# Kernel optimization log

Hardware: AMD Instinct MI355X
Metric: run time of the kernel (lower is better)

Reference implementation:

```python
import jax, jax.numpy as jnp
import numpy as np

B, C, O, N, T, K = 4, 64, 64, 32768, 4, 9
PAD, DIL = 4, 1  # padding*dilation, dilation
SIGMA = 0.05
EPS_BN = 1e-5


def _gather_ch(x, idx):
    # x: [B, C, N], idx: [B, N] -> gather along last dim per channel
    idx3 = jnp.broadcast_to(idx[:, None, :], x.shape)
    return jnp.take_along_axis(x, idx3, axis=-1)


def _weighted_conv(x, coords, w):
    # x: [B,C,N], coords: [B,3,N], w: [O,C,K]
    xp = jnp.pad(x, ((0, 0), (0, 0), (PAD, PAD)))
    cp = jnp.pad(coords, ((0, 0), (0, 0), (PAD, PAD)))
    win_idx = jnp.arange(N)[:, None] + jnp.arange(K) * DIL  # [N, K]
    win = xp[:, :, win_idx]   # [B,C,N,K]
    cwin = cp[:, :, win_idx]  # [B,3,N,K]
    d = cwin - cwin[:, :, :, K // 2:K // 2 + 1]
    s = jnp.sum(d * d, axis=1)                    # [B,N,K]
    r = jnp.sqrt(jnp.where(s > 0, s, 1.0))
    r = jnp.where(s > 0, r, 0.0)
    wgt = jnp.maximum(1.0 - r / SIGMA, 0.0)       # [B,N,K]
    return jnp.einsum('bcnk,bnk,ock->bon', win, wgt, w)


def _bn(x, g, b):
    # training-mode BatchNorm1d over (B, N)
    m = jnp.mean(x, axis=(0, 2), keepdims=True)
    v = jnp.var(x, axis=(0, 2), keepdims=True)
    return g[None, :, None] * (x - m) * jax.lax.rsqrt(v + EPS_BN) + b[None, :, None]


def setup_inputs() -> dict:
    key = jax.random.key(0)
    ks = jax.random.split(key, 12)
    inp = jax.random.normal(ks[0], (B, C, N), dtype=jnp.float32)
    # coords in a small box so sigma=0.05 yields non-trivial weights
    multi_coords = jax.random.uniform(ks[1], (B, 3, N, T), dtype=jnp.float32) * 0.02
    indices = jax.random.randint(ks[2], (B, N, T), 0, N, dtype=jnp.int32)
    reindices = jax.random.randint(ks[3], (B, N, T), 0, N, dtype=jnp.int32)
    fan = C * K
    conv_w = jax.random.normal(ks[4], (T, O, C, K), dtype=jnp.float32) / np.sqrt(fan)
    bn_gamma = jnp.ones((T, O), dtype=jnp.float32)
    bn_beta = jnp.zeros((T, O), dtype=jnp.float32)
    fusion_w = jax.random.normal(ks[5], (O, T * O), dtype=jnp.float32) / np.sqrt(T * O)
    fusion_b = jnp.zeros((O,), dtype=jnp.float32)
    fusion_gamma = jnp.ones((O,), dtype=jnp.float32)
    fusion_beta = jnp.zeros((O,), dtype=jnp.float32)
    return {"input": inp, "multi_coords": multi_coords, "indices": indices,
            "reindices": reindices, "conv_w": conv_w, "bn_gamma": bn_gamma,
            "bn_beta": bn_beta, "fusion_w": fusion_w, "fusion_b": fusion_b,
            "fusion_gamma": fusion_gamma, "fusion_beta": fusion_beta}


def reference(input, multi_coords, indices, reindices, conv_w, bn_gamma, bn_beta,
              fusion_w, fusion_b, fusion_gamma, fusion_beta):
    outs = []
    for i in range(T):  # fixed small set of 4 Hilbert orders
        x = _gather_ch(input, indices[:, :, i])            # [B,C,N]
        x = _weighted_conv(x, multi_coords[:, :, :, i], conv_w[i])  # [B,O,N]
        x = _bn(x, bn_gamma[i], bn_beta[i])
        x = _gather_ch(x, reindices[:, :, i])
        outs.append(x)
    cat = jnp.concatenate(outs, axis=1)                    # [B, T*O, N]
    y = jnp.einsum('bcn,oc->bon', cat, fusion_w) + fusion_b[None, :, None]
    y = _bn(y, fusion_gamma, fusion_beta)
    return jax.nn.relu(y)
```

## Files before the change

### kernel.cpp

```cpp
#include <hip/hip_runtime.h>
#include <hip/hip_bf16.h>

#define BB 4
#define CC 64
#define OO 64
#define NN 32768
#define TT 4
#define KK 9
#define PADW 4
#define SIGMA 0.05f
#define EPS_BN 1e-5f

typedef __attribute__((ext_vector_type(8))) short bf16x8;
typedef __attribute__((ext_vector_type(4))) float f32x4;

__device__ __forceinline__ unsigned short f2bf(float f) {
  __hip_bfloat16 h = __float2bfloat16(f);
  return *reinterpret_cast<unsigned short*>(&h);
}
__device__ __forceinline__ unsigned int pkbf(float a, float b) {
  float2 t; t.x = a; t.y = b;
  __hip_bfloat162 h = __float22bfloat162_rn(t);
  unsigned int r;
  __builtin_memcpy(&r, &h, 4);
  return r;
}

__global__ __launch_bounds__(256) void prep_kernel(
    const float* __restrict__ inp, unsigned short* __restrict__ xTb,
    const float* __restrict__ cw,  unsigned short* __restrict__ W4,
    const int*   __restrict__ ind, const float* __restrict__ mc,
    int* __restrict__ indT, float* __restrict__ mcT)
{
  __shared__ float xt[64][65];
  const int bid = blockIdx.x;
  const int tid = threadIdx.x;

  if (bid < 2048) {
    const int n0 = (bid & 511) * 64;
    const int b  = bid >> 9;
    {
      int nl = tid & 63, c4 = tid >> 6;
      #pragma unroll
      for (int i = 0; i < 16; ++i) {
        int c = c4 * 16 + i;
        xt[c][nl] = inp[((size_t)(b*CC + c))*NN + n0 + nl];
      }
    }
    __syncthreads();
    {
      int nl = tid >> 2, cq = tid & 3;
      unsigned int pk[8];
      #pragma unroll
      for (int i = 0; i < 8; ++i) {
        int c = cq*16 + i*2;
        pk[i] = pkbf(xt[c][nl], xt[c+1][nl]);
      }
      unsigned int* dst = (unsigned int*)(xTb + (((size_t)b*NN) + n0 + nl)*CC + cq*16);
      ((int4*)dst)[0] = make_int4((int)pk[0],(int)pk[1],(int)pk[2],(int)pk[3]);
      ((int4*)dst)[1] = make_int4((int)pk[4],(int)pk[5],(int)pk[6],(int)pk[7]);
    }
  } else if (bid < 2560) {
    const int id = bid - 2048;
    const int n  = (id & 127) * 256 + tid;
    const int b  = id >> 7;
    int4 iv = *(const int4*)(ind + ((size_t)b*NN + n)*TT);
    indT[((size_t)(0*BB + b))*NN + n] = iv.x;
    indT[((size_t)(1*BB + b))*NN + n] = iv.y;
    indT[((size_t)(2*BB + b))*NN + n] = iv.z;
    indT[((size_t)(3*BB + b))*NN + n] = iv.w;
    #pragma unroll
    for (int d = 0; d < 3; ++d) {
      float4 mv = *(const float4*)(mc + (((size_t)(b*3 + d))*NN + n)*TT);
      mcT[((size_t)((0*BB + b)*3 + d))*NN + n] = mv.x;
      mcT[((size_t)((1*BB + b)*3 + d))*NN + n] = mv.y;
      mcT[((size_t)((2*BB + b)*3 + d))*NN + n] = mv.z;
      mcT[((size_t)((3*BB + b)*3 + d))*NN + n] = mv.w;
    }
  } else {
    const int id = bid - 2560;
    const int k = id % KK;
    const int t = id / KK;
    for (int u = tid; u < OO*CC; u += 256) {
      int o = u >> 6, c = u & 63;
      int ow = o >> 5, ot = (o >> 4) & 1, l15 = o & 15;
      int frag = c >> 5, q = (c >> 3) & 3, j = c & 7;
      float wv = cw[(((size_t)(t*OO + o))*CC + c)*KK + k];
      W4[(size_t)(t*9+k)*4096 + ow*2048 + ot*1024 + frag*512 + l15*32 + q*8 + j]
          = f2bf(wv);
    }
  }
}

__global__ __launch_bounds__(256, 3) void conv_kernel(
    const unsigned short* __restrict__ xTb,
    const float* __restrict__ mcT,
    const int*   __restrict__ indT,
    const unsigned short* __restrict__ W4,
    unsigned short* __restrict__ Y,
    float* __restrict__ cpart2)
{
  const int flat = blockIdx.x;
  const int xcd  = flat & 7;
  const int b    = xcd >> 1;
  const int sub  = (xcd & 1) + 2*(flat >> 3);
  const int t    = sub >> 7;
  const int x    = sub & 127;
  const int n0   = x * 256;
  const int tid = threadIdx.x;
  const int lane = tid & 63;
  const int w    = tid >> 6;
  const int l15  = lane & 15;
  const int q    = lane >> 4;
  const int ow   = w & 1;
  const int nw   = w >> 1;

  __shared__ short xg[264*64];
  __shared__ float wgl[256][10];
  __shared__ float mcs[3][268];
  __shared__ int   ids[268];

  for (int u = tid; u < 264; u += 256) {
    int m = n0 + u - PADW;
    bool v = (m >= 0) && (m < NN);
    ids[u] = v ? indT[((size_t)(t*BB + b))*NN + m] : -1;
    #pragma unroll
    for (int d = 0; d < 3; ++d)
      mcs[d][u] = v ? mcT[((size_t)((t*BB + b)*3 + d))*NN + m] : 0.f;
  }
  __syncthreads();

  int4 g[9];
  #pragma unroll
  for (int i = 0; i < 9; ++i) {
    int u = tid + 256*i;
    g[i] = make_int4(0,0,0,0);
    if (u < 2112) {
      int p = u >> 3, s = u & 7;
      int idx = ids[p];
      if (idx >= 0)
        g[i] = *(const int4*)(xTb + ((size_t)b*NN + idx)*CC + s*8);
    }
  }

  {
    int nl = tid;
    float cx = mcs[0][nl+4], cy = mcs[1][nl+4], cz = mcs[2][nl+4];
    #pragma unroll
    for (int k = 0; k < KK; ++k) {
      float dx = mcs[0][nl+k]-cx, dy = mcs[1][nl+k]-cy, dz = mcs[2][nl+k]-cz;
      float s2 = dx*dx + dy*dy + dz*dz;
      float r = (s2 > 0.f) ? sqrtf(s2) : 0.f;
      wgl[nl][k] = fmaxf(1.f - r*(1.f/SIGMA), 0.f);
    }
  }

  #pragma unroll
  for (int i = 0; i < 9; ++i) {
    int u = tid + 256*i;
    if (u < 2112) {
      int p = u >> 3, s = u & 7;
      *(int4*)&xg[(p << 6) + ((s ^ (p & 7)) << 3)] = g[i];
    }
  }
  __syncthreads();

  const unsigned short* Wt = W4 + (size_t)t*9*4096 + ow*2048 + (l15*4 + q)*8;
  const f32x4 Z = {0.f, 0.f, 0.f, 0.f};
  f32x4 fin[2][8];
  #pragma unroll
  for (int ot = 0; ot < 2; ++ot)
    #pragma unroll
    for (int ns = 0; ns < 8; ++ns) fin[ot][ns] = Z;

  for (int k = 0; k < KK; ++k) {
    const unsigned short* Wk = Wt + (size_t)k*4096;
    bf16x8 af[2][2];
    #pragma unroll
    for (int ot = 0; ot < 2; ++ot) {
      af[ot][0] = *(const bf16x8*)(Wk + ot*1024);
      af[ot][1] = *(const bf16x8*)(Wk + ot*1024 + 512);
    }
    #pragma unroll
    for (int ns = 0; ns < 8; ++ns) {
      int nl = nw*128 + ns*16 + l15;
      int p  = nl + k;
      const short* row = &xg[p << 6];
      int sw = p & 7;
      bf16x8 b0 = *(const bf16x8*)(row + ((q ^ sw) << 3));
      bf16x8 b1 = *(const bf16x8*)(row + (((4 + q) ^ sw) << 3));
      float wgt = wgl[nl][k];
      #pragma unroll
      for (int ot = 0; ot < 2; ++ot) {
        f32x4 d = __builtin_amdgcn_mfma_f32_16x16x32_bf16(af[ot][0], b0, Z, 0, 0, 0);
        d = __builtin_amdgcn_mfma_f32_16x16x32_bf16(af[ot][1], b1, d, 0, 0, 0);
        fin[ot][ns] += wgt * d;
      }
    }
  }

  #pragma unroll
  for (int ns = 0; ns < 8; ++ns) {
    int nl = nw*128 + ns*16 + l15;
    size_t row = (((size_t)t*BB + b)*NN + n0 + nl)*OO;
    #pragma unroll
    for (int ot = 0; ot < 2; ++ot) {
      uint2 pk2;
      pk2.x = pkbf(fin[ot][ns][0], fin[ot][ns][1]);
      pk2.y = pkbf(fin[ot][ns][2], fin[ot][ns][3]);
      *(uint2*)(Y + row + ow*32 + ot*16 + q*4) = pk2;
    }
  }

  float sv[16];
  #pragma unroll
  for (int ot = 0; ot < 2; ++ot)
    #pragma unroll
    for (int r = 0; r < 4; ++r) {
      float a = 0.f, qs = 0.f;
      #pragma unroll
      for (int ns = 0; ns < 8; ++ns) {
        float v = fin[ot][ns][r];
        a += v; qs += v*v;
      }
      sv[ot*4+r] = a; sv[8+ot*4+r] = qs;
    }
  #pragma unroll
  for (int msk = 1; msk < 16; msk <<= 1) {
    #pragma unroll
    for (int i = 0; i < 16; ++i) sv[i] += __shfl_xor(sv[i], msk, 16);
  }
  if (l15 == 0) {
    int slot4 = ((b*128 + x) << 2) | w;
    #pragma unroll
    for (int ot = 0; ot < 2; ++ot)
      #pragma unroll
      for (int r = 0; r < 4; ++r) {
        int o = ow*32 + ot*16 + q*4 + r;
        cpart2[((size_t)((t*64 + o)*2 + 0))*2048 + slot4] = sv[ot*4+r];
        cpart2[((size_t)((t*64 + o)*2 + 1))*2048 + slot4] = sv[8+ot*4+r];
      }
  }
}

__global__ __launch_bounds__(256) void bnparam_kernel(
    const float* __restrict__ cpart2,
    const float* __restrict__ gam,
    const float* __restrict__ bet,
    float* __restrict__ ss)
{
  const int to = blockIdx.x;
  const int tid = threadIdx.x;
  __shared__ float r1[256], r2[256];
  const float* p1 = cpart2 + (size_t)to*2*2048;
  const float* p2 = p1 + 2048;
  float s1 = 0.f, s2 = 0.f;
  for (int i = tid*4; i < 2048; i += 1024) {
    float4 a = *(const float4*)(p1 + i);
    float4 c = *(const float4*)(p2 + i);
    s1 += a.x + a.y + a.z + a.w;
    s2 += c.x + c.y + c.z + c.w;
  }
  r1[tid] = s1; r2[tid] = s2;
  __syncthreads();
  for (int st = 128; st > 0; st >>= 1) {
    if (tid < st) { r1[tid] += r1[tid+st]; r2[tid] += r2[tid+st]; }
    __syncthreads();
  }
  if (tid == 0) {
    const float inv = 1.f / (float)(BB * NN);
    float mean = r1[0] * inv;
    float var  = r2[0] * inv - mean * mean;
    float sc = gam[to] * rsqrtf(var + EPS_BN);
    ss[to*2 + 0] = sc;
    ss[to*2 + 1] = bet[to] - mean * sc;
  }
}

__global__ __launch_bounds__(256) void wfuse_kernel(
    const float* __restrict__ fw,
    const float* __restrict__ fb,
    const float* __restrict__ ss,
    float* __restrict__ fbp,
    unsigned short* __restrict__ FWB)
{
  const int tid = threadIdx.x;
  {
    int o = tid >> 2, c0 = (tid & 3) * 64;
    float s = 0.f;
    for (int c = c0; c < c0 + 64; ++c)
      s += fw[o*256 + c] * ss[c*2 + 1];
    s += __shfl_xor(s, 1);
    s += __shfl_xor(s, 2);
    if ((tid & 3) == 0) fbp[o] = fb[o] + s;
  }
  for (int e = tid; e < 16384; e += 256) {
    int rk  = e >> 11;
    int ow  = (e >> 10) & 1;
    int ot  = (e >> 9) & 1;
    int l15 = (e >> 5) & 15;
    int cj  = e & 31;
    int o = ow*32 + ot*16 + l15;
    int c = (rk >> 1)*64 + (rk & 1)*32 + cj;
    FWB[e] = f2bf(fw[o*256 + c] * ss[c*2]);
  }
}

__global__ __launch_bounds__(256, 4) void fusion_kernel(
    const unsigned short* __restrict__ Y,
    const int*   __restrict__ rind,
    const unsigned short* __restrict__ FWB,
    const float* __restrict__ fbp,
    float* __restrict__ out,
    float* __restrict__ fpart2)
{
  const int flat = blockIdx.x;
  const int xcd  = flat & 7;
  const int b    = xcd >> 1;
  const int x    = (xcd & 1) + 2*(flat >> 3);
  const int n0   = x * 128;
  const int tid = threadIdx.x;
  const int lane = tid & 63;
  const int w    = tid >> 6;
  const int l15  = lane & 15;
  const int q    = lane >> 4;
  const int ow   = w & 1;
  const int nw   = w >> 1;

  __shared__ short zg[128*64];

  int4 rg[4];
  #pragma unroll
  for (int i = 0; i < 4; ++i) {
    int n = (tid >> 3) + 32*i;
    rg[i] = *(const int4*)(rind + ((size_t)b*NN + n0 + n)*TT);
  }

  f32x4 fin[2][4];
  #pragma unroll
  for (int ot = 0; ot < 2; ++ot)
    #pragma unroll
    for (int ns = 0; ns < 4; ++ns) fin[ot][ns] = (f32x4){0.f,0.f,0.f,0.f};

  #pragma unroll
  for (int r = 0; r < 4; ++r) {
    if (r) __syncthreads();
    #pragma unroll
    for (int i = 0; i < 4; ++i) {
      int u = tid + 256*i;
      int n = u >> 3, s = u & 7;
      int rn = (r == 0) ? rg[i].x : (r == 1) ? rg[i].y
             : (r == 2) ? rg[i].z : rg[i].w;
      int4 raw = *(const int4*)(Y + (((size_t)r*BB + b)*NN + rn)*OO + s*8);
      *(int4*)&zg[(n << 6) + ((s ^ (n & 7)) << 3)] = raw;
    }
    __syncthreads();

    #pragma unroll
    for (int kk = 0; kk < 2; ++kk) {
      int rk = r*2 + kk;
      const unsigned short* wp = FWB + rk*2048 + ow*1024 + (l15*4 + q)*8;
      bf16x8 af[2];
      af[0] = *(const bf16x8*)(wp);
      af[1] = *(const bf16x8*)(wp + 512);
      #pragma unroll
      for (int ns = 0; ns < 4; ++ns) {
        int nl = nw*64 + ns*16 + l15;
        int ch = (kk*4 + q) ^ (nl & 7);
        bf16x8 bfr = *(const bf16x8*)&zg[(nl << 6) + (ch << 3)];
        #pragma unroll
        for (int ot = 0; ot < 2; ++ot)
          fin[ot][ns] = __builtin_amdgcn_mfma_f32_16x16x32_bf16(af[ot], bfr, fin[ot][ns], 0, 0, 0);
      }
    }
  }

  float sv[16];
  #pragma unroll
  for (int ot = 0; ot < 2; ++ot)
    #pragma unroll
    for (int r2 = 0; r2 < 4; ++r2) {
      int o = ow*32 + ot*16 + q*4 + r2;
      float bias = fbp[o];
      float* dst = out + ((size_t)(b*OO + o))*NN + n0 + nw*64;
      float a = 0.f, qs = 0.f;
      #pragma unroll
      for (int ns = 0; ns < 4; ++ns) {
        float v = fin[ot][ns][r2] + bias;
        dst[ns*16 + l15] = v;
        a += v; qs += v*v;
      }
      sv[ot*4+r2] = a; sv[8+ot*4+r2] = qs;
    }
  #pragma unroll
  for (int msk = 1; msk < 16; msk <<= 1) {
    #pragma unroll
    for (int i = 0; i < 16; ++i) sv[i] += __shfl_xor(sv[i], msk, 16);
  }
  if (l15 == 0) {
    int slot4 = ((b*256 + x) << 2) | w;
    #pragma unroll
    for (int ot = 0; ot < 2; ++ot)
      #pragma unroll
      for (int r2 = 0; r2 < 4; ++r2) {
        int o = ow*32 + ot*16 + q*4 + r2;
        fpart2[((size_t)(o*2 + 0))*4096 + slot4] = sv[ot*4+r2];
        fpart2[((size_t)(o*2 + 1))*4096 + slot4] = sv[8+ot*4+r2];
      }
  }
}

__global__ __launch_bounds__(256) void freduce_kernel(
    const float* __restrict__ fpart2,
    const float* __restrict__ fg,
    const float* __restrict__ fbeta,
    float* __restrict__ fss)
{
  const int o = blockIdx.x;
  const int tid = threadIdx.x;
  __shared__ float r1[256], r2[256];
  const float* p1 = fpart2 + (size_t)o*2*4096;
  const float* p2 = p1 + 4096;
  float s1 = 0.f, s2 = 0.f;
  for (int i = tid*4; i < 4096; i += 1024) {
    float4 a = *(const float4*)(p1 + i);
    float4 c = *(const float4*)(p2 + i);
    s1 += a.x + a.y + a.z + a.w;
    s2 += c.x + c.y + c.z + c.w;
  }
  r1[tid] = s1; r2[tid] = s2;
  __syncthreads();
  for (int st = 128; st > 0; st >>= 1) {
    if (tid < st) { r1[tid] += r1[tid+st]; r2[tid] += r2[tid+st]; }
    __syncthreads();
  }
  if (tid == 0) {
    const float inv = 1.f / (float)(BB * NN);
    float mean = r1[0] * inv;
    float var  = r2[0] * inv - mean * mean;
    float sc = fg[o] * rsqrtf(var + EPS_BN);
    fss[o*2 + 0] = sc;
    fss[o*2 + 1] = fbeta[o] - mean * sc;
  }
}

__global__ __launch_bounds__(256) void final_kernel(
    float* __restrict__ out, const float* __restrict__ fss)
{
  const int base = blockIdx.x * 2048 + threadIdx.x * 4;
  #pragma unroll
  for (int s = 0; s < 2; ++s) {
    int e = base + s * 1024;
    int o2 = (e >> 15) & 63;
    float sc = fss[o2*2 + 0];
    float sh = fss[o2*2 + 1];
    float4 v = *(float4*)(out + e);
    v.x = fmaxf(v.x*sc + sh, 0.f);
    v.y = fmaxf(v.y*sc + sh, 0.f);
    v.z = fmaxf(v.z*sc + sh, 0.f);
    v.w = fmaxf(v.w*sc + sh, 0.f);
    *(float4*)(out + e) = v;
  }
}

extern "C" void kernel_launch(void* const* d_in, const int* in_sizes, int n_in,
                              void* d_out, int out_size, void* d_ws, size_t ws_size,
                              hipStream_t stream) {
  const float* inp  = (const float*)d_in[0];
  const float* mc   = (const float*)d_in[1];
  const int*   ind  = (const int*)  d_in[2];
  const int*   rind = (const int*)  d_in[3];
  const float* cw   = (const float*)d_in[4];
  const float* bg   = (const float*)d_in[5];
  const float* bb   = (const float*)d_in[6];
  const float* fw   = (const float*)d_in[7];
  const float* fb   = (const float*)d_in[8];
  const float* fg   = (const float*)d_in[9];
  const float* fbt  = (const float*)d_in[10];

  char* ws = (char*)d_ws;
  float* convss = (float*)(ws + 0);
  float* fss    = (float*)(ws + 2048);
  float* fbp    = (float*)(ws + 3072);
  unsigned short* Y = (unsigned short*)(ws + 8192);
  float* fpart2 = (float*)(ws + 8192 + 67108864);
  unsigned short* FWB = (unsigned short*)(ws + 8192 + 67108864 + 2097152);

  char* ob = (char*)d_out;
  unsigned short* xTb = (unsigned short*)ob;
  unsigned short* W4  = (unsigned short*)(ob + 16777216);
  float* cpart2 = (float*)(ob + 17072128);
  int*   indT   = (int*)  (ob + 21266432);
  float* mcT    = (float*)(ob + 23363584);
  float* out = (float*)d_out;

  prep_kernel<<<2596, 256, 0, stream>>>(inp, xTb, cw, W4, ind, mc, indT, mcT);

  conv_kernel<<<2048, 256, 0, stream>>>(xTb, mcT, indT, W4, Y, cpart2);

  bnparam_kernel<<<256, 256, 0, stream>>>(cpart2, bg, bb, convss);

  wfuse_kernel<<<1, 256, 0, stream>>>(fw, fb, convss, fbp, FWB);

  fusion_kernel<<<1024, 256, 0, stream>>>(Y, rind, FWB, fbp, out, fpart2);

  freduce_kernel<<<OO, 256, 0, stream>>>(fpart2, fg, fbt, fss);

  final_kernel<<<(BB*OO*NN)/2048, 256, 0, stream>>>(out, fss);
}
```

Before: 213.1 us.

## Restructure conv kernel into independent per-wave 64-point tiles without block barriers

The conv kernel now launches 128-thread blocks in which each wave owns its own 64-point tile and computes all 64 output channels, rather than four waves sharing a 256-point tile split by output half. Each wave stages its own indices, coordinates and gathered features in private shared memory, so the __syncthreads barriers become compiler memory fences. The aim is to remove block-wide synchronisation stalls and raise occupancy through smaller blocks. In exchange, the halo overhead per point grows (72 rows staged for 64 points instead of 264 for 256), each wave holds more accumulators and twice the weight fragments in registers, and intra-wave LDS ordering rests on the wave running in lockstep.

```diff
diff --git a/kernel.cpp b/kernel.cpp
--- a/kernel.cpp
+++ b/kernel.cpp
@@ -92,7 +92,7 @@
   }
 }
 
-__global__ __launch_bounds__(256, 3) void conv_kernel(
+__global__ __launch_bounds__(128, 3) void conv_kernel(
     const unsigned short* __restrict__ xTb,
     const float* __restrict__ mcT,
     const int*   __restrict__ indT,
@@ -104,141 +104,134 @@
   const int xcd  = flat & 7;
   const int b    = xcd >> 1;
   const int sub  = (xcd & 1) + 2*(flat >> 3);
-  const int t    = sub >> 7;
-  const int x    = sub & 127;
-  const int n0   = x * 256;
-  const int tid = threadIdx.x;
+  const int t    = sub >> 8;
+  const int x    = sub & 255;
+  const int tid  = threadIdx.x;
   const int lane = tid & 63;
   const int w    = tid >> 6;
+  const int n0w  = x*128 + w*64;
   const int l15  = lane & 15;
   const int q    = lane >> 4;
-  const int ow   = w & 1;
-  const int nw   = w >> 1;
-
-  __shared__ short xg[264*64];
-  __shared__ float wgl[256][10];
-  __shared__ float mcs[3][268];
-  __shared__ int   ids[268];
-
-  for (int u = tid; u < 264; u += 256) {
-    int m = n0 + u - PADW;
+
+  __shared__ short xg[2][72*64];
+  __shared__ float wgl[2][64][10];
+  __shared__ float mcs[2][3][72];
+  __shared__ int   ids[2][72];
+
+  for (int u = lane; u < 72; u += 64) {
+    int m = n0w + u - PADW;
     bool v = (m >= 0) && (m < NN);
-    ids[u] = v ? indT[((size_t)(t*BB + b))*NN + m] : -1;
+    ids[w][u] = v ? indT[((size_t)(t*BB + b))*NN + m] : -1;
     #pragma unroll
     for (int d = 0; d < 3; ++d)
-      mcs[d][u] = v ? mcT[((size_t)((t*BB + b)*3 + d))*NN + m] : 0.f;
-  }
-  __syncthreads();
+      mcs[w][d][u] = v ? mcT[((size_t)((t*BB + b)*3 + d))*NN + m] : 0.f;
+  }
+  asm volatile("" ::: "memory");
 
   int4 g[9];
   #pragma unroll
   for (int i = 0; i < 9; ++i) {
-    int u = tid + 256*i;
+    int u = lane + 64*i;
+    int p = u >> 3, s = u & 7;
+    int idx = ids[w][p];
     g[i] = make_int4(0,0,0,0);
-    if (u < 2112) {
-      int p = u >> 3, s = u & 7;
-      int idx = ids[p];
-      if (idx >= 0)
-        g[i] = *(const int4*)(xTb + ((size_t)b*NN + idx)*CC + s*8);
-    }
+    if (idx >= 0)
+      g[i] = *(const int4*)(xTb + ((size_t)b*NN + idx)*CC + s*8);
   }
 
   {
-    int nl = tid;
-    float cx = mcs[0][nl+4], cy = mcs[1][nl+4], cz = mcs[2][nl+4];
+    int nl = lane;
+    float cx = mcs[w][0][nl+4], cy = mcs[w][1][nl+4], cz = mcs[w][2][nl+4];
     #pragma unroll
     for (int k = 0; k < KK; ++k) {
-      float dx = mcs[0][nl+k]-cx, dy = mcs[1][nl+k]-cy, dz = mcs[2][nl+k]-cz;
+      float dx = mcs[w][0][nl+k]-cx, dy = mcs[w][1][nl+k]-cy, dz = mcs[w][2][nl+k]-cz;
       float s2 = dx*dx + dy*dy + dz*dz;
       float r = (s2 > 0.f) ? sqrtf(s2) : 0.f;
-      wgl[nl][k] = fmaxf(1.f - r*(1.f/SIGMA), 0.f);
+      wgl[w][nl][k] = fmaxf(1.f - r*(1.f/SIGMA), 0.f);
     }
   }
 
   #pragma unroll
   for (int i = 0; i < 9; ++i) {
-    int u = tid + 256*i;
-    if (u < 2112) {
-      int p = u >> 3, s = u & 7;
-      *(int4*)&xg[(p << 6) + ((s ^ (p & 7)) << 3)] = g[i];
-    }
-  }
-  __syncthreads();
-
-  const unsigned short* Wt = W4 + (size_t)t*9*4096 + ow*2048 + (l15*4 + q)*8;
+    int u = lane + 64*i;
+    int p = u >> 3, s = u & 7;
+    *(int4*)&xg[w][(p << 6) + ((s ^ (p & 7)) << 3)] = g[i];
+  }
+  asm volatile("" ::: "memory");
+
+  const unsigned short* Wt = W4 + (size_t)t*9*4096 + (l15*4 + q)*8;
   const f32x4 Z = {0.f, 0.f, 0.f, 0.f};
-  f32x4 fin[2][8];
-  #pragma unroll
-  for (int ot = 0; ot < 2; ++ot)
-    #pragma unroll
-    for (int ns = 0; ns < 8; ++ns) fin[ot][ns] = Z;
+  f32x4 fin[4][4];
+  #pragma unroll
+  for (int j = 0; j < 4; ++j)
+    #pragma unroll
+    for (int ns = 0; ns < 4; ++ns) fin[j][ns] = Z;
 
   for (int k = 0; k < KK; ++k) {
     const unsigned short* Wk = Wt + (size_t)k*4096;
-    bf16x8 af[2][2];
-    #pragma unroll
-    for (int ot = 0; ot < 2; ++ot) {
-      af[ot][0] = *(const bf16x8*)(Wk + ot*1024);
-      af[ot][1] = *(const bf16x8*)(Wk + ot*1024 + 512);
-    }
-    #pragma unroll
-    for (int ns = 0; ns < 8; ++ns) {
-      int nl = nw*128 + ns*16 + l15;
+    bf16x8 af[4][2];
+    #pragma unroll
+    for (int j = 0; j < 4; ++j) {
+      af[j][0] = *(const bf16x8*)(Wk + j*1024);
+      af[j][1] = *(const bf16x8*)(Wk + j*1024 + 512);
+    }
+    #pragma unroll
+    for (int ns = 0; ns < 4; ++ns) {
+      int nl = ns*16 + l15;
       int p  = nl + k;
-      const short* row = &xg[p << 6];
+      const short* row = &xg[w][p << 6];
       int sw = p & 7;
       bf16x8 b0 = *(const bf16x8*)(row + ((q ^ sw) << 3));
       bf16x8 b1 = *(const bf16x8*)(row + (((4 + q) ^ sw) << 3));
-      float wgt = wgl[nl][k];
-      #pragma unroll
-      for (int ot = 0; ot < 2; ++ot) {
-        f32x4 d = __builtin_amdgcn_mfma_f32_16x16x32_bf16(af[ot][0], b0, Z, 0, 0, 0);
-        d = __builtin_amdgcn_mfma_f32_16x16x32_bf16(af[ot][1], b1, d, 0, 0, 0);
-        fin[ot][ns] += wgt * d;
-      }
-    }
-  }
-
-  #pragma unroll
-  for (int ns = 0; ns < 8; ++ns) {
-    int nl = nw*128 + ns*16 + l15;
-    size_t row = (((size_t)t*BB + b)*NN + n0 + nl)*OO;
-    #pragma unroll
-    for (int ot = 0; ot < 2; ++ot) {
+      float wgt = wgl[w][nl][k];
+      #pragma unroll
+      for (int j = 0; j < 4; ++j) {
+        f32x4 d = __builtin_amdgcn_mfma_f32_16x16x32_bf16(af[j][0], b0, Z, 0, 0, 0);
+        d = __builtin_amdgcn_mfma_f32_16x16x32_bf16(af[j][1], b1, d, 0, 0, 0);
+        fin[j][ns] += wgt * d;
+      }
+    }
+  }
+
+  #pragma unroll
+  for (int ns = 0; ns < 4; ++ns) {
+    size_t row = (((size_t)t*BB + b)*NN + n0w + ns*16 + l15)*OO;
+    #pragma unroll
+    for (int j = 0; j < 4; ++j) {
       uint2 pk2;
-      pk2.x = pkbf(fin[ot][ns][0], fin[ot][ns][1]);
-      pk2.y = pkbf(fin[ot][ns][2], fin[ot][ns][3]);
-      *(uint2*)(Y + row + ow*32 + ot*16 + q*4) = pk2;
-    }
-  }
-
-  float sv[16];
-  #pragma unroll
-  for (int ot = 0; ot < 2; ++ot)
+      pk2.x = pkbf(fin[j][ns][0], fin[j][ns][1]);
+      pk2.y = pkbf(fin[j][ns][2], fin[j][ns][3]);
+      *(uint2*)(Y + row + j*16 + q*4) = pk2;
+    }
+  }
+
+  float sv[32];
+  #pragma unroll
+  for (int j = 0; j < 4; ++j)
     #pragma unroll
     for (int r = 0; r < 4; ++r) {
       float a = 0.f, qs = 0.f;
       #pragma unroll
-      for (int ns = 0; ns < 8; ++ns) {
-        float v = fin[ot][ns][r];
+      for (int ns = 0; ns < 4; ++ns) {
+        float v = fin[j][ns][r];
         a += v; qs += v*v;
       }
-      sv[ot*4+r] = a; sv[8+ot*4+r] = qs;
+      sv[j*4+r] = a; sv[16+j*4+r] = qs;
     }
   #pragma unroll
   for (int msk = 1; msk < 16; msk <<= 1) {
     #pragma unroll
-    for (int i = 0; i < 16; ++i) sv[i] += __shfl_xor(sv[i], msk, 16);
+    for (int i = 0; i < 32; ++i) sv[i] += __shfl_xor(sv[i], msk, 16);
   }
   if (l15 == 0) {
-    int slot4 = ((b*128 + x) << 2) | w;
-    #pragma unroll
-    for (int ot = 0; ot < 2; ++ot)
+    int slot = ((b*256 + x) << 1) | w;
+    #pragma unroll
+    for (int j = 0; j < 4; ++j)
       #pragma unroll
       for (int r = 0; r < 4; ++r) {
-        int o = ow*32 + ot*16 + q*4 + r;
-        cpart2[((size_t)((t*64 + o)*2 + 0))*2048 + slot4] = sv[ot*4+r];
-        cpart2[((size_t)((t*64 + o)*2 + 1))*2048 + slot4] = sv[8+ot*4+r];
+        int o = j*16 + q*4 + r;
+        cpart2[((size_t)((t*64 + o)*2 + 0))*2048 + slot] = sv[j*4+r];
+        cpart2[((size_t)((t*64 + o)*2 + 1))*2048 + slot] = sv[16+j*4+r];
       }
   }
 }
@@ -496,7 +489,7 @@
 
   prep_kernel<<<2596, 256, 0, stream>>>(inp, xTb, cw, W4, ind, mc, indT, mcT);
 
-  conv_kernel<<<2048, 256, 0, stream>>>(xTb, mcT, indT, W4, Y, cpart2);
+  conv_kernel<<<4096, 128, 0, stream>>>(xTb, mcT, indT, W4, Y, cpart2);
 
   bnparam_kernel<<<256, 256, 0, stream>>>(cpart2, bg, bb, convss);
 
```

Result: slower. 226.4 us (+6.3%).
